# Optimization experiments

Hardware: AMD Instinct MI355X
Metric: run time of the kernel (lower is better)

Reference implementation:

```python
import jax, jax.numpy as jnp
import numpy as np

X_SCALE = 20.0
THR = 0.25
BETA = 15.0
DT = 1.0
GAIN = 1.0


def setup_inputs() -> dict:
    key = jax.random.key(0)
    k1, k2, k3 = jax.random.split(key, 3)
    x = jax.random.normal(k1, (32, 1, 8192), dtype=jnp.float32)
    conv_w = jax.random.normal(k2, (64, 1, 8), dtype=jnp.float32)
    raw_tau = jax.random.normal(k3, (64,), dtype=jnp.float32)
    return {"x": x, "conv_w": conv_w, "raw_tau": raw_tau}


def _forward(x, conv_w, raw_tau):
    K = conv_w.shape[-1]
    # normalize each filter to unit norm (clamp_min 1e-8)
    norms = jnp.linalg.norm(conv_w.reshape(conv_w.shape[0], -1), axis=1)
    w = conv_w / jnp.maximum(norms, 1e-8)[:, None, None]
    # causal conv: left-pad by K-1
    I = GAIN * jax.lax.conv_general_dilated(
        X_SCALE * x, w, window_strides=(1,), padding=[(K - 1, 0)],
        dimension_numbers=("NCH", "OIH", "NCH"))  # (B, F, L)
    tau = jax.nn.softplus(raw_tau) + 1e-4
    alpha = jnp.exp(-DT / tau).astype(I.dtype)  # (F,)

    def step(v, I_t):
        v_pre = alpha * v + (1.0 - alpha) * I_t  # (B, F)
        z = BETA * (v_pre - THR)
        s = (v_pre >= THR).astype(I_t.dtype)  # hard spike, no grad
        v_new = v_pre * (1.0 - s)  # reset where spiked
        return v_new, (z, s)

    I_tfirst = jnp.transpose(I, (2, 0, 1))  # (L, B, F)
    v0 = jnp.zeros(I.shape[:2], dtype=I.dtype)  # (B, F)
    _, (z, s) = jax.lax.scan(step, v0, I_tfirst)
    z = jnp.transpose(z, (1, 2, 0))  # (B, F, L)
    s = jnp.transpose(s, (1, 2, 0))
    logits = jnp.max(z, axis=1)  # (B, L)
    return I, z, s, logits


def reference(x, conv_w, raw_tau):
    return _forward(x, conv_w, raw_tau)
```

## Files before the change

### kernel.cpp

```cpp
#include <hip/hip_runtime.h>
#include <math.h>


#define LL 8192
#define BB 32
#define FF 64
#define KK 8
#define CHUNK 128
#define NCH 64
#define WARM 96
#define NX (WARM + 7 + CHUNK)
#define TS 32
#define NT (CHUNK / TS)

__global__ __launch_bounds__(64) void snn_kernel(
    const float* __restrict__ x, const float* __restrict__ conv_w,
    const float* __restrict__ raw_tau, float* __restrict__ out)
{
    __shared__ double x_lds[NX + 1];
    __shared__ float I_tile[FF][TS + 1];
    __shared__ float z_tile[FF][TS + 1];

    const int f  = threadIdx.x;
    const int b  = blockIdx.y;
    const int c  = blockIdx.x;
    const int t0 = c * CHUNK;
    const int g0 = t0 - WARM - 7;

    double wd[KK];
    double ss = 0.0;
    #pragma unroll
    for (int k = 0; k < KK; ++k) {
        double wv = (double)conv_w[f * KK + k];
        wd[k] = wv;
        ss += wv * wv;
    }
    double nrm = sqrt(ss);
    if (nrm < 1e-8) nrm = 1e-8;
    double invn = 1.0 / nrm;
    #pragma unroll
    for (int k = 0; k < KK; ++k) wd[k] *= invn;

    double rt    = (double)raw_tau[f];
    double tau   = log1p(exp(rt)) + 1e-4;
    double alpha = exp(-1.0 / tau);
    double oma   = 1.0 - alpha;

    for (int i = f; i < NX; i += 64) {
        int g = g0 + i;
        x_lds[i] = (g >= 0) ? (double)(20.0f * x[(size_t)b * LL + g]) : 0.0;
    }

    float* outI  = out;
    float* outZ  = out + (size_t)BB * FF * LL;
    float* outS  = out + (size_t)2 * BB * FF * LL;
    float* outLg = out + (size_t)3 * BB * FF * LL;

    double v = 0.0;

    #pragma unroll 8
    for (int s = 0; s < WARM; ++s) {
        double acc = 0.0;
        #pragma unroll
        for (int k = 0; k < KK; ++k) acc = fma(wd[k], x_lds[s + k], acc);
        double vp = fma(alpha, v, oma * acc);
        v = (vp >= 0.25) ? 0.0 : vp;
    }

    for (int tile = 0; tile < NT; ++tile) {
        #pragma unroll
        for (int j = 0; j < TS; ++j) {
            int s = WARM + tile * TS + j;
            double acc = 0.0;
            #pragma unroll
            for (int k = 0; k < KK; ++k) acc = fma(wd[k], x_lds[s + k], acc);
            double vp = fma(alpha, v, oma * acc);
            double z  = 15.0 * (vp - 0.25);
            I_tile[f][j] = (float)acc;
            z_tile[f][j] = (float)z;
            v = (vp >= 0.25) ? 0.0 : vp;
        }

        const int gt = t0 + tile * TS;
        {
            int r = f >> 3;
            int q = (f & 7) * 4;
            #pragma unroll
            for (int it = 0; it < 8; ++it) {
                int fr = it * 8 + r;
                size_t base = ((size_t)b * FF + fr) * LL + gt + q;
                float4 vi = make_float4(I_tile[fr][q], I_tile[fr][q + 1],
                                        I_tile[fr][q + 2], I_tile[fr][q + 3]);
                float4 vz = make_float4(z_tile[fr][q], z_tile[fr][q + 1],
                                        z_tile[fr][q + 2], z_tile[fr][q + 3]);
                float4 vs = make_float4(vz.x >= 0.f ? 1.f : 0.f,
                                        vz.y >= 0.f ? 1.f : 0.f,
                                        vz.z >= 0.f ? 1.f : 0.f,
                                        vz.w >= 0.f ? 1.f : 0.f);
                *reinterpret_cast<float4*>(outI + base) = vi;
                *reinterpret_cast<float4*>(outZ + base) = vz;
                *reinterpret_cast<float4*>(outS + base) = vs;
            }
            if (f < TS) {
                float m = z_tile[0][f];
                #pragma unroll
                for (int ff = 1; ff < FF; ++ff) m = fmaxf(m, z_tile[ff][f]);
                outLg[(size_t)b * LL + gt + f] = m;
            }
        }
    }
}

extern "C" void kernel_launch(void* const* d_in, const int* in_sizes, int n_in,
                              void* d_out, int out_size, void* d_ws, size_t ws_size,
                              hipStream_t stream) {
    const float* x  = (const float*)d_in[0];
    const float* w  = (const float*)d_in[1];
    const float* rt = (const float*)d_in[2];
    float* out = (float*)d_out;
    dim3 grid(NCH, BB);
    snn_kernel<<<grid, 64, 0, stream>>>(x, w, rt, out);
}
```

Measured before the change: 206.7 us.

## Switch recurrence to fp32, use nontemporal stores, split logits max across lanes

Moves the convolution and leaky-integrate recurrence from double to float arithmetic, using float LDS for x. Output tiles are written with nontemporal vector stores to avoid cache pollution. The per-timestep max over filters is split across both halves of the wavefront and combined with a shuffle, so all 64 lanes share the work instead of 32. Fp32 accumulation may flip spike decisions near the threshold relative to the reference.

```diff
diff --git a/kernel.cpp b/kernel.cpp
--- a/kernel.cpp
+++ b/kernel.cpp
@@ -13,11 +13,13 @@
 #define TS 32
 #define NT (CHUNK / TS)
 
+typedef float f32x4 __attribute__((ext_vector_type(4)));
+
 __global__ __launch_bounds__(64) void snn_kernel(
     const float* __restrict__ x, const float* __restrict__ conv_w,
     const float* __restrict__ raw_tau, float* __restrict__ out)
 {
-    __shared__ double x_lds[NX + 1];
+    __shared__ float x_lds[NX + 1];
     __shared__ float I_tile[FF][TS + 1];
     __shared__ float z_tile[FF][TS + 1];
 
@@ -27,28 +29,30 @@
     const int t0 = c * CHUNK;
     const int g0 = t0 - WARM - 7;
 
-    double wd[KK];
+    double wdd[KK];
     double ss = 0.0;
     #pragma unroll
     for (int k = 0; k < KK; ++k) {
         double wv = (double)conv_w[f * KK + k];
-        wd[k] = wv;
+        wdd[k] = wv;
         ss += wv * wv;
     }
     double nrm = sqrt(ss);
     if (nrm < 1e-8) nrm = 1e-8;
     double invn = 1.0 / nrm;
+    float wf[KK];
     #pragma unroll
-    for (int k = 0; k < KK; ++k) wd[k] *= invn;
+    for (int k = 0; k < KK; ++k) wf[k] = (float)(wdd[k] * invn);
 
-    double rt    = (double)raw_tau[f];
-    double tau   = log1p(exp(rt)) + 1e-4;
-    double alpha = exp(-1.0 / tau);
-    double oma   = 1.0 - alpha;
+    double rt     = (double)raw_tau[f];
+    double tau    = log1p(exp(rt)) + 1e-4;
+    double alphad = exp(-1.0 / tau);
+    float alpha = (float)alphad;
+    float oma   = (float)(1.0 - alphad);
 
     for (int i = f; i < NX; i += 64) {
         int g = g0 + i;
-        x_lds[i] = (g >= 0) ? (double)(20.0f * x[(size_t)b * LL + g]) : 0.0;
+        x_lds[i] = (g >= 0) ? (20.0f * x[(size_t)b * LL + g]) : 0.0f;
     }
 
     float* outI  = out;
@@ -56,29 +60,29 @@
     float* outS  = out + (size_t)2 * BB * FF * LL;
     float* outLg = out + (size_t)3 * BB * FF * LL;
 
-    double v = 0.0;
+    float v = 0.0f;
 
     #pragma unroll 8
     for (int s = 0; s < WARM; ++s) {
-        double acc = 0.0;
+        float acc = 0.0f;
         #pragma unroll
-        for (int k = 0; k < KK; ++k) acc = fma(wd[k], x_lds[s + k], acc);
-        double vp = fma(alpha, v, oma * acc);
-        v = (vp >= 0.25) ? 0.0 : vp;
+        for (int k = 0; k < KK; ++k) acc = fmaf(wf[k], x_lds[s + k], acc);
+        float vp = fmaf(alpha, v, oma * acc);
+        v = (vp >= 0.25f) ? 0.0f : vp;
     }
 
     for (int tile = 0; tile < NT; ++tile) {
         #pragma unroll
         for (int j = 0; j < TS; ++j) {
             int s = WARM + tile * TS + j;
-            double acc = 0.0;
+            float acc = 0.0f;
             #pragma unroll
-            for (int k = 0; k < KK; ++k) acc = fma(wd[k], x_lds[s + k], acc);
-            double vp = fma(alpha, v, oma * acc);
-            double z  = 15.0 * (vp - 0.25);
-            I_tile[f][j] = (float)acc;
-            z_tile[f][j] = (float)z;
-            v = (vp >= 0.25) ? 0.0 : vp;
+            for (int k = 0; k < KK; ++k) acc = fmaf(wf[k], x_lds[s + k], acc);
+            float vp = fmaf(alpha, v, oma * acc);
+            float z  = fmaf(15.0f, vp, -3.75f);
+            I_tile[f][j] = acc;
+            z_tile[f][j] = z;
+            v = (vp >= 0.25f) ? 0.0f : vp;
         }
 
         const int gt = t0 + tile * TS;
@@ -89,24 +93,24 @@
             for (int it = 0; it < 8; ++it) {
                 int fr = it * 8 + r;
                 size_t base = ((size_t)b * FF + fr) * LL + gt + q;
-                float4 vi = make_float4(I_tile[fr][q], I_tile[fr][q + 1],
-                                        I_tile[fr][q + 2], I_tile[fr][q + 3]);
-                float4 vz = make_float4(z_tile[fr][q], z_tile[fr][q + 1],
-                                        z_tile[fr][q + 2], z_tile[fr][q + 3]);
-                float4 vs = make_float4(vz.x >= 0.f ? 1.f : 0.f,
-                                        vz.y >= 0.f ? 1.f : 0.f,
-                                        vz.z >= 0.f ? 1.f : 0.f,
-                                        vz.w >= 0.f ? 1.f : 0.f);
-                *reinterpret_cast<float4*>(outI + base) = vi;
-                *reinterpret_cast<float4*>(outZ + base) = vz;
-                *reinterpret_cast<float4*>(outS + base) = vs;
+                f32x4 vi = { I_tile[fr][q], I_tile[fr][q + 1],
+                             I_tile[fr][q + 2], I_tile[fr][q + 3] };
+                f32x4 vz = { z_tile[fr][q], z_tile[fr][q + 1],
+                             z_tile[fr][q + 2], z_tile[fr][q + 3] };
+                f32x4 vs = { vz.x >= 0.f ? 1.f : 0.f,
+                             vz.y >= 0.f ? 1.f : 0.f,
+                             vz.z >= 0.f ? 1.f : 0.f,
+                             vz.w >= 0.f ? 1.f : 0.f };
+                __builtin_nontemporal_store(vi, reinterpret_cast<f32x4*>(outI + base));
+                __builtin_nontemporal_store(vz, reinterpret_cast<f32x4*>(outZ + base));
+                __builtin_nontemporal_store(vs, reinterpret_cast<f32x4*>(outS + base));
             }
-            if (f < TS) {
-                float m = z_tile[0][f];
-                #pragma unroll
-                for (int ff = 1; ff < FF; ++ff) m = fmaxf(m, z_tile[ff][f]);
-                outLg[(size_t)b * LL + gt + f] = m;
-            }
+            int t = f & 31, g = f >> 5;
+            float m = z_tile[g * 32][t];
+            #pragma unroll
+            for (int i = 1; i < 32; ++i) m = fmaxf(m, z_tile[g * 32 + i][t]);
+            m = fmaxf(m, __shfl_xor(m, 32));
+            if (f < 32) outLg[(size_t)b * LL + gt + f] = m;
         }
     }
 }
```

Result: slower. 215.6 us (+4.3%).
